# Kernel optimization log

Hardware: AMD Instinct MI355X
Metric: run time of the kernel (lower is better)

Reference implementation:

```python
import jax, jax.numpy as jnp
import numpy as np

NX = 2048
NY = 2048
LINK_LEN = 100.0  # uniform link length (m)

RHO_W, RHO_I, G = 1000.0, 917.0, 9.81
SEC_PER_A = 31556926.0
K_S, A_S = 0.01, 1.25          # sheet conductivity / flow exponent
K_C, A_C = 0.1, 3.0            # channel conductivity / flow exponent
H_R, L_C = 0.1, 2.0            # bedrock step height / cavity spacing
A_CL, N_GLEN = 5e-25, 3        # closure coeff / Glen exponent
C_T, C_W = 7.5e-8, 4220.0      # pressure-melt coeff / heat capacity


def _build_grid(nx, ny):
    ids = np.arange(nx * ny, dtype=np.int32).reshape(ny, nx)
    # links: tail -> head, horizontal then vertical
    h_tail = ids[:, :-1].ravel(); h_head = ids[:, 1:].ravel()
    v_tail = ids[:-1, :].ravel(); v_head = ids[1:, :].ravel()
    tail = np.concatenate([h_tail, v_tail]); head = np.concatenate([h_head, v_head])
    adj = np.full((ny, nx, 4), -1, dtype=np.int32)
    adj[:, 1:, 0] = ids[:, :-1]   # left
    adj[:, :-1, 1] = ids[:, 1:]   # right
    adj[1:, :, 2] = ids[:-1, :]   # down
    adj[:-1, :, 3] = ids[1:, :]   # up
    status = np.zeros((ny, nx), dtype=np.int32)
    status[0, :] = status[-1, :] = 1
    status[:, 0] = status[:, -1] = 1
    return head, tail, adj.reshape(-1, 4), status.ravel()


def setup_inputs() -> dict:
    key = jax.random.key(0)
    ks = jax.random.split(key, 6)
    head, tail, adj, status = _build_grid(NX, NY)
    N = NX * NY
    L = head.shape[0]
    bedrock = jax.random.uniform(ks[0], (N,), dtype=jnp.float32) * 500.0
    ice_thickness = jax.random.uniform(ks[1], (N,), dtype=jnp.float32) * 1000.0 + 100.0
    base = RHO_W * G * bedrock
    overburden = base + RHO_I * G * ice_thickness
    potential = base + 0.8 * (overburden - base) + jax.random.normal(ks[2], (N,), dtype=jnp.float32) * 1e3
    sheet_thickness = jax.random.uniform(ks[3], (N,), dtype=jnp.float32) * 0.2
    channel_size = jax.random.uniform(ks[4], (L,), dtype=jnp.float32) * 2.0
    sliding_velocity = jax.random.normal(ks[5], (L,), dtype=jnp.float32) * 50.0  # m/a on links
    return dict(
        potential=potential,
        sheet_thickness=sheet_thickness,
        channel_size=channel_size,
        bedrock_elevation=bedrock,
        ice_thickness=ice_thickness,
        sliding_velocity=sliding_velocity,
        node_at_link_head=jnp.asarray(head),
        node_at_link_tail=jnp.asarray(tail),
        adjacent_nodes_at_node=jnp.asarray(adj),
        status_at_node=jnp.asarray(status),
    )


def reference(potential, sheet_thickness, channel_size, bedrock_elevation, ice_thickness,
              sliding_velocity, node_at_link_head, node_at_link_tail,
              adjacent_nodes_at_node, status_at_node):
    head, tail = node_at_link_head, node_at_link_tail
    n_nodes = potential.shape[0]

    base = RHO_W * G * bedrock_elevation                       # base_potential
    overburden = base + RHO_I * G * ice_thickness              # overburden_potential

    grad = (potential[head] - potential[tail]) / LINK_LEN      # calc_grad_at_link
    flow_direction = jnp.where(potential[head] > potential[tail], -1, 1)

    # set_inflow_outflow
    adj = adjacent_nodes_at_node
    max_adj = jnp.max(jnp.where(adj != -1, potential[adj], -jnp.inf), axis=1)
    boundary = (status_at_node > 0).astype(jnp.int32)
    inflow_outflow = jnp.where(potential > max_adj, boundary, -boundary)

    water_pressure = potential - base
    eff_N = overburden - potential

    # sheet / channel discharge on links
    h_link = 0.5 * (sheet_thickness[head] + sheet_thickness[tail])
    sheet_q = -K_S * h_link ** A_S * jnp.abs(grad) ** (-0.5) * grad
    channel_q = -K_C * channel_size ** A_C * grad

    # calc_sheet_opening: mean of |u_b|/sec_per_a over links at each node
    u = jnp.abs(sliding_velocity) / SEC_PER_A
    seg = jnp.concatenate([head, tail])
    val = jnp.concatenate([u, u])
    num = jax.ops.segment_sum(val, seg, num_segments=n_nodes)
    cnt = jax.ops.segment_sum(jnp.ones_like(val), seg, num_segments=n_nodes)
    sliding_node = num / jnp.maximum(cnt, 1.0)
    opening = jnp.where(sheet_thickness < H_R,
                        sliding_node * (H_R - sheet_thickness) / L_C, 0.0)

    relu = lambda x: jnp.where(x > 0.0, x, 0.0)
    sheet_closure = A_CL * sheet_thickness * relu(eff_N) ** N_GLEN
    N_link = 0.5 * (eff_N[head] + eff_N[tail])
    channel_closure = A_CL * channel_size * relu(N_link) ** N_GLEN

    dissipation = jnp.abs(channel_q * grad) + jnp.abs(L_C * sheet_q * grad)

    p_grad = (water_pressure[head] - water_pressure[tail]) / LINK_LEN
    total_q = jnp.where((channel_size > 0) | (p_grad * sheet_q > 0),
                        channel_q + L_C * sheet_q, channel_q)
    sensible = (-C_T * C_W * RHO_W) * total_q * p_grad

    return (flow_direction, inflow_outflow, sheet_q, channel_q, opening,
            sheet_closure, channel_closure, dissipation, sensible)
```

## Files before the change

kernel.cpp:

```cpp
#include <hip/hip_runtime.h>
#include <math.h>

constexpr int NXc = 2048;
constexpr int NYc = 2048;
constexpr int LH   = NYc * (NXc - 1);
constexpr int LV   = (NYc - 1) * NXc;
constexpr int LTOT = LH + LV;
constexpr int NN   = NXc * NYc;

constexpr int OFF_FDIR  = 0;
constexpr int OFF_IO    = LTOT;
constexpr int OFF_SQ    = LTOT + NN;
constexpr int OFF_CQ    = 2 * LTOT + NN;
constexpr int OFF_OPEN  = 3 * LTOT + NN;
constexpr int OFF_SCL   = 3 * LTOT + 2 * NN;
constexpr int OFF_CCL   = 3 * LTOT + 3 * NN;
constexpr int OFF_DISS  = 4 * LTOT + 3 * NN;
constexpr int OFF_SENS  = 5 * LTOT + 3 * NN;

__global__ __launch_bounds__(256) void sgd_kernel(
    const float* __restrict__ pot,
    const float* __restrict__ sheet,
    const float* __restrict__ csz,
    const float* __restrict__ bed,
    const float* __restrict__ ice,
    const float* __restrict__ sv,
    const int*   __restrict__ status,
    float* __restrict__ out)
{
    constexpr float RWG    = 9810.0f;
    constexpr float RIG    = 8995.77f;
    constexpr float INV_L  = 0.01f;
    constexpr float KS     = 0.01f;
    constexpr float KC     = 0.1f;
    constexpr float ACL    = 5e-25f;
    constexpr float SEC_A  = 31556926.0f;
    constexpr float SENS_C = 0.3165f;

    const int wg    = blockIdx.x;
    const int chunk = (int)gridDim.x >> 3;
    const int swz   = (wg & 7) * chunk + (wg >> 3);
    const int idx   = swz * 256 + (int)threadIdx.x;

    if (idx < LTOT) {
        int ht, hh;
        if (idx < LH) {
            int y = idx / (NXc - 1);
            int x = idx - y * (NXc - 1);
            ht = y * NXc + x;
            hh = ht + 1;
        } else {
            ht = idx - LH;
            hh = ht + NXc;
        }

        const float pt = pot[ht],   ph = pot[hh];
        const float st = sheet[ht], sh = sheet[hh];
        const float bt = bed[ht],   bh = bed[hh];
        const float it = ice[ht],   ih = ice[hh];
        const float cs = __builtin_nontemporal_load(&csz[idx]);

        const float grad = (ph - pt) * INV_L;
        const float fdir = (ph > pt) ? -1.0f : 1.0f;

        const float base_t = RWG * bt,            base_h = RWG * bh;
        const float ob_t   = base_t + RIG * it,   ob_h   = base_h + RIG * ih;
        const float wp_t   = pt - base_t,         wp_h   = ph - base_h;
        const float eN_t   = ob_t - pt,           eN_h   = ob_h - ph;

        const float hl = 0.5f * (sh + st);
        const float ag = fabsf(grad);
        const float hp = hl * sqrtf(sqrtf(hl));
        const float sq = -KS * hp * (grad * rsqrtf(ag));
        const float cq = -KC * (cs * cs * cs) * grad;

        const float Nl  = 0.5f * (eN_h + eN_t);
        const float rc  = fmaxf(Nl, 0.0f);
        const float ccl = ACL * cs * (rc * rc * rc);

        const float diss = fabsf(cq * grad) + fabsf(2.0f * sq * grad);

        const float pg = (wp_h - wp_t) * INV_L;
        const float tq = ((cs > 0.0f) || (pg * sq > 0.0f)) ? (cq + 2.0f * sq) : cq;
        const float sens = -SENS_C * tq * pg;

        __builtin_nontemporal_store(fdir, &out[OFF_FDIR + idx]);
        __builtin_nontemporal_store(sq,   &out[OFF_SQ   + idx]);
        __builtin_nontemporal_store(cq,   &out[OFF_CQ   + idx]);
        __builtin_nontemporal_store(ccl,  &out[OFF_CCL  + idx]);
        __builtin_nontemporal_store(diss, &out[OFF_DISS + idx]);
        __builtin_nontemporal_store(sens, &out[OFF_SENS + idx]);
    } else {
        const int n = idx - LTOT;
        const int y = n >> 11;
        const int x = n & (NXc - 1);

        const float p = pot[n];
        float mx = -INFINITY;
        if (x > 0)       mx = fmaxf(mx, pot[n - 1]);
        if (x < NXc - 1) mx = fmaxf(mx, pot[n + 1]);
        if (y > 0)       mx = fmaxf(mx, pot[n - NXc]);
        if (y < NYc - 1) mx = fmaxf(mx, pot[n + NXc]);

        const int  st_n = __builtin_nontemporal_load(&status[n]);
        const float bfl = (st_n > 0) ? 1.0f : 0.0f;
        const float io  = (p > mx) ? bfl : -bfl;

        float usum = 0.0f, cnt = 0.0f;
        if (x > 0)       { usum += fabsf(sv[y * (NXc - 1) + (x - 1)]) / SEC_A; cnt += 1.0f; }
        if (x < NXc - 1) { usum += fabsf(sv[y * (NXc - 1) + x])       / SEC_A; cnt += 1.0f; }
        if (y > 0)       { usum += fabsf(sv[LH + n - NXc])            / SEC_A; cnt += 1.0f; }
        if (y < NYc - 1) { usum += fabsf(sv[LH + n])                  / SEC_A; cnt += 1.0f; }
        const float snode = usum / cnt;

        const float sh_n = sheet[n];
        const float opening = (sh_n < 0.1f) ? (snode * (0.1f - sh_n) * 0.5f) : 0.0f;

        const float eN = (RWG * bed[n] + RIG * ice[n]) - p;
        const float r  = fmaxf(eN, 0.0f);
        const float scl = ACL * sh_n * (r * r * r);

        __builtin_nontemporal_store(io,      &out[OFF_IO   + n]);
        __builtin_nontemporal_store(opening, &out[OFF_OPEN + n]);
        __builtin_nontemporal_store(scl,     &out[OFF_SCL  + n]);
    }
}

extern "C" void kernel_launch(void* const* d_in, const int* in_sizes, int n_in,
                              void* d_out, int out_size, void* d_ws, size_t ws_size,
                              hipStream_t stream) {
    const float* pot    = (const float*)d_in[0];
    const float* sheet  = (const float*)d_in[1];
    const float* csz    = (const float*)d_in[2];
    const float* bed    = (const float*)d_in[3];
    const float* ice    = (const float*)d_in[4];
    const float* sv     = (const float*)d_in[5];
    const int*   status = (const int*)d_in[9];
    float* out = (float*)d_out;

    const int total  = LTOT + NN;
    const int blocks = total / 256;
    sgd_kernel<<<blocks, 256, 0, stream>>>(pot, sheet, csz, bed, ice, sv, status, out);
}
```

Before: 509.0 us.

## Process four elements per thread with 128-bit vector loads and stores

Each thread now handles four consecutive links or nodes, using float4 loads for node fields and float4 stores for outputs, and reuses neighbouring values within a register window instead of reloading them. The block swizzle and nontemporal hints are removed, and the grid shrinks fourfold. This targets memory-instruction count and redundant gathers in a bandwidth-bound kernel. The cost is higher register pressure, unaligned loads on horizontal links, and per-element row-boundary selects.

```diff
diff --git a/kernel.cpp b/kernel.cpp
--- a/kernel.cpp
+++ b/kernel.cpp
@@ -1,5 +1,8 @@
 #include <hip/hip_runtime.h>
 #include <math.h>
+
+using f4  = float __attribute__((ext_vector_type(4)));
+using i4v = int   __attribute__((ext_vector_type(4)));
 
 constexpr int NXc = 2048;
 constexpr int NYc = 2048;
@@ -7,6 +10,11 @@
 constexpr int LV   = (NYc - 1) * NXc;
 constexpr int LTOT = LH + LV;
 constexpr int NN   = NXc * NYc;
+
+constexpr int TH   = LH / 4;
+constexpr int TV   = LV / 4;
+constexpr int TN   = NN / 4;
+constexpr int TTOT = TH + TV + TN;
 
 constexpr int OFF_FDIR  = 0;
 constexpr int OFF_IO    = LTOT;
@@ -17,6 +25,54 @@
 constexpr int OFF_CCL   = 3 * LTOT + 3 * NN;
 constexpr int OFF_DISS  = 4 * LTOT + 3 * NN;
 constexpr int OFF_SENS  = 5 * LTOT + 3 * NN;
+
+constexpr float RWG    = 9810.0f;
+constexpr float RIG    = 8995.77f;
+constexpr float INV_L  = 0.01f;
+constexpr float KS     = 0.01f;
+constexpr float KC     = 0.1f;
+constexpr float ACL    = 5e-25f;
+constexpr float SEC_A  = 31556926.0f;
+constexpr float SENS_C = 0.3165f;
+
+__device__ inline f4 load4u(const float* p) {
+    f4 v; __builtin_memcpy(&v, p, sizeof(v)); return v;
+}
+__device__ inline f4 load4a(const float* p) { return *(const f4*)p; }
+__device__ inline void store4(float* p, f4 v) { *(f4*)p = v; }
+
+struct LinkOut { float fdir, sq, cq, ccl, diss, sens; };
+
+__device__ inline LinkOut link_compute(float pt, float ph, float st, float sh,
+                                       float bt, float bh, float it, float ih,
+                                       float cs)
+{
+    LinkOut o;
+    const float grad = (ph - pt) * INV_L;
+    o.fdir = (ph > pt) ? -1.0f : 1.0f;
+
+    const float base_t = RWG * bt,          base_h = RWG * bh;
+    const float eN_t   = base_t + RIG * it - pt;
+    const float eN_h   = base_h + RIG * ih - ph;
+    const float wp_t   = pt - base_t,       wp_h   = ph - base_h;
+
+    const float hl = 0.5f * (sh + st);
+    const float ag = fabsf(grad);
+    const float hp = hl * sqrtf(sqrtf(hl));
+    o.sq = -KS * hp * (grad * rsqrtf(ag));
+    o.cq = -KC * (cs * cs * cs) * grad;
+
+    const float Nl = 0.5f * (eN_h + eN_t);
+    const float rc = fmaxf(Nl, 0.0f);
+    o.ccl = ACL * cs * (rc * rc * rc);
+
+    o.diss = fabsf(o.cq * grad) + fabsf(2.0f * o.sq * grad);
+
+    const float pg = (wp_h - wp_t) * INV_L;
+    const float tq = ((cs > 0.0f) || (pg * o.sq > 0.0f)) ? (o.cq + 2.0f * o.sq) : o.cq;
+    o.sens = -SENS_C * tq * pg;
+    return o;
+}
 
 __global__ __launch_bounds__(256) void sgd_kernel(
     const float* __restrict__ pot,
@@ -28,101 +84,127 @@
     const int*   __restrict__ status,
     float* __restrict__ out)
 {
-    constexpr float RWG    = 9810.0f;
-    constexpr float RIG    = 8995.77f;
-    constexpr float INV_L  = 0.01f;
-    constexpr float KS     = 0.01f;
-    constexpr float KC     = 0.1f;
-    constexpr float ACL    = 5e-25f;
-    constexpr float SEC_A  = 31556926.0f;
-    constexpr float SENS_C = 0.3165f;
-
-    const int wg    = blockIdx.x;
-    const int chunk = (int)gridDim.x >> 3;
-    const int swz   = (wg & 7) * chunk + (wg >> 3);
-    const int idx   = swz * 256 + (int)threadIdx.x;
-
-    if (idx < LTOT) {
-        int ht, hh;
-        if (idx < LH) {
-            int y = idx / (NXc - 1);
-            int x = idx - y * (NXc - 1);
-            ht = y * NXc + x;
-            hh = ht + 1;
-        } else {
-            ht = idx - LH;
-            hh = ht + NXc;
+    const int tid = blockIdx.x * 256 + (int)threadIdx.x;
+
+    if (tid < TH) {
+        const int l0 = tid * 4;
+        const int y0 = l0 / 2047;
+        const int b  = (y0 + 1) * 2047;
+        const int t0 = l0 + y0;
+        const int i5 = (t0 + 5 < NN) ? t0 + 5 : 0;
+
+        const f4 pw = load4u(pot + t0);   const float pe4 = pot[t0+4],   pe5 = pot[i5];
+        const f4 sw = load4u(sheet + t0); const float se4 = sheet[t0+4], se5 = sheet[i5];
+        const f4 bw = load4u(bed + t0);   const float be4 = bed[t0+4],   be5 = bed[i5];
+        const f4 iw = load4u(ice + t0);   const float ie4 = ice[t0+4],   ie5 = ice[i5];
+        const f4 c4 = load4a(csz + l0);
+
+        const float pa[6] = {pw[0],pw[1],pw[2],pw[3],pe4,pe5};
+        const float sa[6] = {sw[0],sw[1],sw[2],sw[3],se4,se5};
+        const float ba[6] = {bw[0],bw[1],bw[2],bw[3],be4,be5};
+        const float ia[6] = {iw[0],iw[1],iw[2],iw[3],ie4,ie5};
+
+        f4 o_f, o_sq, o_cq, o_ccl, o_d, o_se;
+        #pragma unroll
+        for (int i = 0; i < 4; ++i) {
+            const bool dy = (l0 + i >= b);
+            const float pt = dy ? pa[i+1] : pa[i], ph = dy ? pa[i+2] : pa[i+1];
+            const float st = dy ? sa[i+1] : sa[i], sh = dy ? sa[i+2] : sa[i+1];
+            const float bt = dy ? ba[i+1] : ba[i], bh = dy ? ba[i+2] : ba[i+1];
+            const float it = dy ? ia[i+1] : ia[i], ih = dy ? ia[i+2] : ia[i+1];
+            const LinkOut o = link_compute(pt, ph, st, sh, bt, bh, it, ih, c4[i]);
+            o_f[i] = o.fdir; o_sq[i] = o.sq; o_cq[i] = o.cq;
+            o_ccl[i] = o.ccl; o_d[i] = o.diss; o_se[i] = o.sens;
         }
-
-        const float pt = pot[ht],   ph = pot[hh];
-        const float st = sheet[ht], sh = sheet[hh];
-        const float bt = bed[ht],   bh = bed[hh];
-        const float it = ice[ht],   ih = ice[hh];
-        const float cs = __builtin_nontemporal_load(&csz[idx]);
-
-        const float grad = (ph - pt) * INV_L;
-        const float fdir = (ph > pt) ? -1.0f : 1.0f;
-
-        const float base_t = RWG * bt,            base_h = RWG * bh;
-        const float ob_t   = base_t + RIG * it,   ob_h   = base_h + RIG * ih;
-        const float wp_t   = pt - base_t,         wp_h   = ph - base_h;
-        const float eN_t   = ob_t - pt,           eN_h   = ob_h - ph;
-
-        const float hl = 0.5f * (sh + st);
-        const float ag = fabsf(grad);
-        const float hp = hl * sqrtf(sqrtf(hl));
-        const float sq = -KS * hp * (grad * rsqrtf(ag));
-        const float cq = -KC * (cs * cs * cs) * grad;
-
-        const float Nl  = 0.5f * (eN_h + eN_t);
-        const float rc  = fmaxf(Nl, 0.0f);
-        const float ccl = ACL * cs * (rc * rc * rc);
-
-        const float diss = fabsf(cq * grad) + fabsf(2.0f * sq * grad);
-
-        const float pg = (wp_h - wp_t) * INV_L;
-        const float tq = ((cs > 0.0f) || (pg * sq > 0.0f)) ? (cq + 2.0f * sq) : cq;
-        const float sens = -SENS_C * tq * pg;
-
-        __builtin_nontemporal_store(fdir, &out[OFF_FDIR + idx]);
-        __builtin_nontemporal_store(sq,   &out[OFF_SQ   + idx]);
-        __builtin_nontemporal_store(cq,   &out[OFF_CQ   + idx]);
-        __builtin_nontemporal_store(ccl,  &out[OFF_CCL  + idx]);
-        __builtin_nontemporal_store(diss, &out[OFF_DISS + idx]);
-        __builtin_nontemporal_store(sens, &out[OFF_SENS + idx]);
+        store4(out + OFF_FDIR + l0, o_f);
+        store4(out + OFF_SQ   + l0, o_sq);
+        store4(out + OFF_CQ   + l0, o_cq);
+        store4(out + OFF_CCL  + l0, o_ccl);
+        store4(out + OFF_DISS + l0, o_d);
+        store4(out + OFF_SENS + l0, o_se);
+    } else if (tid < TH + TV) {
+        const int k0 = (tid - TH) * 4;
+        const int l0 = LH + k0;
+
+        const f4 pt = load4a(pot + k0),   ph = load4a(pot + k0 + NXc);
+        const f4 st = load4a(sheet + k0), sh = load4a(sheet + k0 + NXc);
+        const f4 bt = load4a(bed + k0),   bh = load4a(bed + k0 + NXc);
+        const f4 it = load4a(ice + k0),   ih = load4a(ice + k0 + NXc);
+        const f4 c4 = load4a(csz + l0);
+
+        f4 o_f, o_sq, o_cq, o_ccl, o_d, o_se;
+        #pragma unroll
+        for (int i = 0; i < 4; ++i) {
+            const LinkOut o = link_compute(pt[i], ph[i], st[i], sh[i],
+                                           bt[i], bh[i], it[i], ih[i], c4[i]);
+            o_f[i] = o.fdir; o_sq[i] = o.sq; o_cq[i] = o.cq;
+            o_ccl[i] = o.ccl; o_d[i] = o.diss; o_se[i] = o.sens;
+        }
+        store4(out + OFF_FDIR + l0, o_f);
+        store4(out + OFF_SQ   + l0, o_sq);
+        store4(out + OFF_CQ   + l0, o_cq);
+        store4(out + OFF_CCL  + l0, o_ccl);
+        store4(out + OFF_DISS + l0, o_d);
+        store4(out + OFF_SENS + l0, o_se);
     } else {
-        const int n = idx - LTOT;
-        const int y = n >> 11;
-        const int x = n & (NXc - 1);
-
-        const float p = pot[n];
-        float mx = -INFINITY;
-        if (x > 0)       mx = fmaxf(mx, pot[n - 1]);
-        if (x < NXc - 1) mx = fmaxf(mx, pot[n + 1]);
-        if (y > 0)       mx = fmaxf(mx, pot[n - NXc]);
-        if (y < NYc - 1) mx = fmaxf(mx, pot[n + NXc]);
-
-        const int  st_n = __builtin_nontemporal_load(&status[n]);
-        const float bfl = (st_n > 0) ? 1.0f : 0.0f;
-        const float io  = (p > mx) ? bfl : -bfl;
-
-        float usum = 0.0f, cnt = 0.0f;
-        if (x > 0)       { usum += fabsf(sv[y * (NXc - 1) + (x - 1)]) / SEC_A; cnt += 1.0f; }
-        if (x < NXc - 1) { usum += fabsf(sv[y * (NXc - 1) + x])       / SEC_A; cnt += 1.0f; }
-        if (y > 0)       { usum += fabsf(sv[LH + n - NXc])            / SEC_A; cnt += 1.0f; }
-        if (y < NYc - 1) { usum += fabsf(sv[LH + n])                  / SEC_A; cnt += 1.0f; }
-        const float snode = usum / cnt;
-
-        const float sh_n = sheet[n];
-        const float opening = (sh_n < 0.1f) ? (snode * (0.1f - sh_n) * 0.5f) : 0.0f;
-
-        const float eN = (RWG * bed[n] + RIG * ice[n]) - p;
-        const float r  = fmaxf(eN, 0.0f);
-        const float scl = ACL * sh_n * (r * r * r);
-
-        __builtin_nontemporal_store(io,      &out[OFF_IO   + n]);
-        __builtin_nontemporal_store(opening, &out[OFF_OPEN + n]);
-        __builtin_nontemporal_store(scl,     &out[OFF_SCL  + n]);
+        const int n0 = (tid - TH - TV) * 4;
+        const int y  = n0 >> 11;
+        const int x0 = n0 & (NXc - 1);
+
+        const f4  p4 = load4a(pot + n0);
+        const float pm1 = pot[n0 - (x0 > 0 ? 1 : 0)];
+        const float pp4 = pot[n0 + (x0 < NXc - 4 ? 4 : 0)];
+        const f4  pu = load4a(pot + (y > 0        ? n0 - NXc : n0));
+        const f4  pd = load4a(pot + (y < NYc - 1  ? n0 + NXc : n0));
+        const f4  s4 = load4a(sheet + n0);
+        const f4  b4 = load4a(bed + n0);
+        const f4  ic4 = load4a(ice + n0);
+        const i4v st4 = *(const i4v*)(status + n0);
+
+        const int hb = y * (NXc - 1) + x0;
+        const float Wm1 = sv[hb > 0 ? hb - 1 : 0];
+        const f4  Wv  = load4u(sv + hb);
+        const f4  vu  = load4a(sv + LH + n0 - NXc + (y > 0 ? 0 : NXc));
+        const f4  vd  = load4a(sv + LH + (y < NYc - 1 ? n0 : 0));
+
+        f4 o_io, o_op, o_sc;
+        #pragma unroll
+        for (int i = 0; i < 4; ++i) {
+            const int  x    = x0 + i;
+            const bool hasL = (x > 0), hasR = (x < NXc - 1);
+            const bool hasU = (y > 0), hasD = (y < NYc - 1);
+            const float p = p4[i];
+
+            const float PL = (i == 0) ? pm1 : p4[i - 1 < 0 ? 0 : i - 1];
+            const float PR = (i == 3) ? pp4 : p4[i + 1 > 3 ? 3 : i + 1];
+
+            float mx = hasL ? PL : -INFINITY;
+            mx = fmaxf(mx, hasR ? PR     : -INFINITY);
+            mx = fmaxf(mx, hasU ? pu[i]  : -INFINITY);
+            mx = fmaxf(mx, hasD ? pd[i]  : -INFINITY);
+
+            const float bfl = (st4[i] > 0) ? 1.0f : 0.0f;
+            o_io[i] = (p > mx) ? bfl : -bfl;
+
+            const float svL = (i == 0) ? Wm1 : Wv[i - 1 < 0 ? 0 : i - 1];
+            const float svR = Wv[i];
+            float usum = 0.0f, cnt = 0.0f;
+            if (hasL) { usum += fabsf(svL)   / SEC_A; cnt += 1.0f; }
+            if (hasR) { usum += fabsf(svR)   / SEC_A; cnt += 1.0f; }
+            if (hasU) { usum += fabsf(vu[i]) / SEC_A; cnt += 1.0f; }
+            if (hasD) { usum += fabsf(vd[i]) / SEC_A; cnt += 1.0f; }
+            const float snode = usum / cnt;
+
+            const float shn = s4[i];
+            o_op[i] = (shn < 0.1f) ? (snode * (0.1f - shn) * 0.5f) : 0.0f;
+
+            const float eN = (RWG * b4[i] + RIG * ic4[i]) - p;
+            const float r  = fmaxf(eN, 0.0f);
+            o_sc[i] = ACL * shn * (r * r * r);
+        }
+        store4(out + OFF_IO   + n0, o_io);
+        store4(out + OFF_OPEN + n0, o_op);
+        store4(out + OFF_SCL  + n0, o_sc);
     }
 }
 
@@ -138,7 +220,6 @@
     const int*   status = (const int*)d_in[9];
     float* out = (float*)d_out;
 
-    const int total  = LTOT + NN;
-    const int blocks = total / 256;
+    const int blocks = TTOT / 256;
     sgd_kernel<<<blocks, 256, 0, stream>>>(pot, sheet, csz, bed, ice, sv, status, out);
 }
```

New measurement: 437.3 us. -14.1%, faster.
